# Kernel optimization log

Measured on AMD Instinct MI355X. Metric: run time of the kernel, lower is better.

Reference implementation:

```python
import jax, jax.numpy as jnp
import numpy as np

NUM_NODES = 100000
NUM_EDGES = 1600000
DIM = 64
TAU = 0.5
EPS = 1e-12
SURGERY_EPS = 1e-6


def setup_inputs() -> dict:
    key = jax.random.key(0)
    k1, k2, k3, k4, k5 = jax.random.split(key, 5)
    x = jax.random.normal(k1, (NUM_NODES, DIM), dtype=jnp.float32)
    edge_index = jax.random.randint(k2, (2, NUM_EDGES), 0, NUM_NODES, dtype=jnp.int64)
    edge_weight = jax.random.uniform(k3, (NUM_EDGES,), dtype=jnp.float32)
    # nn.Linear weights (no bias): y = x @ W.T
    W_self = jax.random.normal(k4, (DIM, DIM), dtype=jnp.float32) / np.sqrt(DIM)
    W_neigh = jax.random.normal(k5, (DIM, DIM), dtype=jnp.float32) / np.sqrt(DIM)
    return {"x": x, "edge_index": edge_index, "edge_weight": edge_weight,
            "W_self": W_self, "W_neigh": W_neigh}


def reference(x, edge_index, edge_weight, W_self, W_neigh):
    num_nodes = x.shape[0]
    row, col = edge_index[0], edge_index[1]

    # --- Ollivier-Ricci (LLY limit-free combinatorial lower-bound) curvature per edge ---
    deg = jax.ops.segment_sum(edge_weight, row, num_segments=num_nodes)  # weighted out-degree
    inv_du = 1.0 / jnp.maximum(deg[row], EPS)
    inv_dv = 1.0 / jnp.maximum(deg[col], EPS)
    kappa = 2.0 * inv_du + 2.0 * inv_dv - 2.0  # [E]

    # --- CFL-stable step size for the Ricci flow ---
    delta_t = 0.5 / (jnp.max(jnp.abs(kappa)) + 1e-6)

    # --- Ricci-flow half step: dw/dt = -kappa * w ---
    w_half = jnp.maximum(edge_weight * (1.0 - 0.5 * delta_t * kappa), 0.0)

    # --- metric surgery: drop degenerate edges (implemented as a zero-weight mask,
    #     keeping edge count static so the kernel is jit-compatible) ---
    mask = w_half > SURGERY_EPS
    w_half = jnp.where(mask, w_half, 0.0)

    # --- row normalisation ---
    row_sum = jax.ops.segment_sum(w_half, row, num_segments=num_nodes)
    w_norm = w_half / jnp.maximum(row_sum[row], EPS)

    # --- Laplacian off-diagonals: L_uv = -w_norm  =>  -L_uv = w_norm ---
    minus_L = w_norm

    # --- incident mean curvature per node (over surviving edges) -> curvature gate ---
    cnt = jax.ops.segment_sum(mask.astype(x.dtype), row, num_segments=num_nodes)
    k_sum = jax.ops.segment_sum(jnp.where(mask, kappa, 0.0), row, num_segments=num_nodes)
    mean_kappa = k_sum / jnp.maximum(cnt, 1.0)
    rho = jax.nn.sigmoid(mean_kappa)  # [N]

    # --- gated message passing ---
    h_self = x @ W_self.T    # [N, D]
    h_neigh = x @ W_neigh.T  # [N, D]
    msg = minus_L[:, None] * h_neigh[col]                      # [E, D] gather + scale
    neigh_aggr = jax.ops.segment_sum(msg, row, num_segments=num_nodes)  # scatter-add

    # h0 buffer == first-forward x (detached)
    out = rho[:, None] * h_self + neigh_aggr + TAU * x
    return out, edge_index, w_norm
```

## Files before the change

### kernel.cpp

```cpp
#include <hip/hip_runtime.h>
#include <math.h>

#define NNODES 100000
#define NEDGES 1600000
#define DIM 64
#define TAU 0.5f
#define EPSF 1e-12f
#define SEPS 1e-6f

#define K 256
#define RPB 391
#define TILE 8192
#define CAP 7168

typedef unsigned long long ull;
typedef unsigned short u16;
typedef __attribute__((ext_vector_type(8))) short bf16x8;
typedef __attribute__((ext_vector_type(4))) float f32x4;

__device__ __forceinline__ float bf2f(u16 h) {
    return __uint_as_float((unsigned)h << 16);
}
__device__ __forceinline__ u16 f2bf(float f) {
    unsigned u = __float_as_uint(f);
    u += 0x7FFFu + ((u >> 16) & 1);
    return (u16)(u >> 16);
}

__global__ __launch_bounds__(256) void k_bcount(const int* __restrict__ ei,
                                                int* __restrict__ bcnt, int E, int N) {
    __shared__ int cnt[K];
    cnt[threadIdx.x] = 0;
    __syncthreads();
    int stride = gridDim.x * blockDim.x;
    for (int e = blockIdx.x * blockDim.x + threadIdx.x; e < E; e += stride) {
        int r = min(max(ei[e], 0), N - 1);
        atomicAdd(&cnt[r / RPB], 1);
    }
    __syncthreads();
    int v = cnt[threadIdx.x];
    if (v) atomicAdd(&bcnt[threadIdx.x], v);
}

__global__ __launch_bounds__(256) void k_bscan(const int* __restrict__ bcnt,
                                               int* __restrict__ bbase, int* __restrict__ bcur,
                                               int* __restrict__ off, int E, int N) {
    __shared__ int sc[K];
    int t = threadIdx.x;
    int v = bcnt[t];
    sc[t] = v;
    __syncthreads();
    for (int o = 1; o < K; o <<= 1) {
        int a = (t >= o) ? sc[t - o] : 0;
        __syncthreads();
        sc[t] += a;
        __syncthreads();
    }
    int ex = sc[t] - v;
    bbase[t] = ex;
    bcur[t] = ex;
    if (t == K - 1) { bbase[K] = sc[t]; off[N] = E; }
}

__global__ __launch_bounds__(256) void k_bin(const int* __restrict__ ei, const float* __restrict__ w,
                                             int* __restrict__ bcur, ull* __restrict__ arena,
                                             int E, int N) {
    __shared__ ull stg[TILE];
    __shared__ int cnt[K], lscan[K], gbase[K], cur[K], sc[K];
    int t = threadIdx.x;
    int e0 = blockIdx.x * TILE;
    cnt[t] = 0; cur[t] = 0;
    __syncthreads();
    for (int i = t; i < TILE; i += 256) {
        int e = e0 + i;
        if (e < E) {
            int r = min(max(ei[e], 0), N - 1);
            atomicAdd(&cnt[r / RPB], 1);
        }
    }
    __syncthreads();
    int v = cnt[t];
    sc[t] = v;
    __syncthreads();
    for (int o = 1; o < K; o <<= 1) {
        int a = (t >= o) ? sc[t - o] : 0;
        __syncthreads();
        sc[t] += a;
        __syncthreads();
    }
    lscan[t] = sc[t] - v;
    if (v > 0) gbase[t] = atomicAdd(&bcur[t], v);
    __syncthreads();
    for (int i = t; i < TILE; i += 256) {
        int e = e0 + i;
        if (e < E) {
            int r = min(max(ei[e], 0), N - 1);
            int c = min(max(ei[E + e], 0), N - 1);
            int b = r / RPB, lr = r - b * RPB;
            int p = lscan[b] + atomicAdd(&cur[b], 1);
            stg[p] = ((ull)__float_as_uint(w[e]) << 32) | (unsigned)(c | (lr << 17));
        }
    }
    __syncthreads();
    int nb = cnt[t];
    if (nb > 0) {
        int src = lscan[t];
        size_t dst = (size_t)gbase[t];
        for (int j = 0; j < nb; j++) arena[dst + j] = stg[src + j];
    }
}

__global__ __launch_bounds__(256) void k_sort(const int* __restrict__ bbase,
                                              ull* __restrict__ arena,
                                              float* __restrict__ invdeg,
                                              int* __restrict__ off, int N) {
    __shared__ ull stg[CAP];
    __shared__ int hist[RPB];
    __shared__ float degl[RPB];
    __shared__ int cur[RPB];
    __shared__ int sc[512];
    int t = threadIdx.x, b = blockIdx.x;
    int base = bbase[b];
    int cnt = min(bbase[b + 1] - base, CAP);
    for (int i = t; i < RPB; i += 256) { hist[i] = 0; degl[i] = 0.0f; cur[i] = 0; }
    __syncthreads();
    for (int i = t; i < cnt; i += 256) {
        ull rec = arena[base + i];
        stg[i] = rec;
        int lr = (int)((rec >> 17) & 0x1FF);
        atomicAdd(&hist[lr], 1);
        atomicAdd(&degl[lr], __uint_as_float((unsigned)(rec >> 32)));
    }
    __syncthreads();
    int v0 = (t < RPB) ? hist[t] : 0;
    int v1 = (t + 256 < RPB) ? hist[t + 256] : 0;
    sc[t] = v0; sc[t + 256] = v1;
    __syncthreads();
    for (int o = 1; o < 512; o <<= 1) {
        int a = (t >= o) ? sc[t - o] : 0;
        int c2 = (t + 256 >= o) ? sc[t + 256 - o] : 0;
        __syncthreads();
        sc[t] += a; sc[t + 256] += c2;
        __syncthreads();
    }
    int ex0 = sc[t] - v0, ex1 = sc[t + 256] - v1;
    hist[t] = ex0;
    if (t + 256 < RPB) hist[t + 256] = ex1;
    int rn0 = b * RPB + t;
    if (rn0 < N) { off[rn0] = base + ex0; invdeg[rn0] = 1.0f / fmaxf(degl[t], EPSF); }
    int rn1 = rn0 + 256;
    if (t + 256 < RPB && rn1 < N) { off[rn1] = base + ex1; invdeg[rn1] = 1.0f / fmaxf(degl[t + 256], EPSF); }
    __syncthreads();
    int2* out2 = (int2*)arena;
    for (int i = t; i < cnt; i += 256) {
        ull rec = stg[i];
        int lr = (int)((rec >> 17) & 0x1FF);
        int p = hist[lr] + atomicAdd(&cur[lr], 1);
        out2[base + p] = make_int2((int)(rec & 0x1FFFF), (int)(unsigned)(rec >> 32));
    }
}

__global__ __launch_bounds__(256) void k_maxk(const int* __restrict__ off, const int2* __restrict__ csr,
                                              const float* __restrict__ invdeg,
                                              float* __restrict__ maxabs, int N) {
    int n = blockIdx.x * 256 + threadIdx.x;
    float m = 0.0f;
    if (n < N) {
        int s = off[n], e = off[n + 1];
        float a = 2.0f * invdeg[n] - 2.0f;
        for (int i = s; i < e; i++) {
            int2 pr = csr[i];
            m = fmaxf(m, fabsf(a + 2.0f * invdeg[pr.x]));
        }
    }
    for (int o = 32; o > 0; o >>= 1) m = fmaxf(m, __shfl_down(m, o, 64));
    __shared__ float red[4];
    int lane = threadIdx.x & 63, wid = threadIdx.x >> 6;
    if (lane == 0) red[wid] = m;
    __syncthreads();
    if (threadIdx.x == 0) {
        float bm = fmaxf(fmaxf(red[0], red[1]), fmaxf(red[2], red[3]));
        atomicMax((unsigned int*)maxabs, __float_as_uint(bm));
    }
}

__global__ void k_node(const int* __restrict__ off, const float* __restrict__ invdeg,
                       int2* __restrict__ csr, const float* __restrict__ maxabs,
                       float* __restrict__ rho, float* __restrict__ row_sum, int N) {
    int n = blockIdx.x * blockDim.x + threadIdx.x;
    if (n >= N) return;
    int s = off[n], e2 = off[n + 1];
    float dt = 0.5f / (*maxabs + 1e-6f);
    float a = 2.0f * invdeg[n] - 2.0f;
    float rs = 0.0f, ct = 0.0f, ks = 0.0f;
    for (int i = s; i < e2; i++) {
        int2 pr = csr[i];
        float we = __int_as_float(pr.y);
        float kap = a + 2.0f * invdeg[pr.x];
        float wh = fmaxf(we * (1.0f - 0.5f * dt * kap), 0.0f);
        float wst = 0.0f;
        if (wh > SEPS) { rs += wh; ct += 1.0f; ks += kap; wst = wh; }
        csr[i] = make_int2(pr.x, __float_as_int(wst));
    }
    float mk = ks / fmaxf(ct, 1.0f);
    rho[n] = 1.0f / (1.0f + expf(-mk));
    row_sum[n] = rs;
}

#define WL(mp, d, kk) (((mp) * 64 + (d)) * 72 + (kk))
__global__ __launch_bounds__(256) void k_gemm(const float* __restrict__ x,
                                              const float* __restrict__ Wself,
                                              const float* __restrict__ Wneigh,
                                              const float* __restrict__ rho,
                                              u16* __restrict__ hneigh_h,
                                              float* __restrict__ out, int N) {
    __shared__ u16 wlds[4 * 64 * 72];
    int t = threadIdx.x;
    for (int i = t; i < 4096; i += 256) {
        int d = i >> 6, k = i & 63;
        float v = Wself[i];
        u16 h = f2bf(v);
        u16 lo = f2bf(v - bf2f(h));
        wlds[WL(0, d, k)] = h;
        wlds[WL(1, d, k)] = lo;
        v = Wneigh[i];
        h = f2bf(v);
        lo = f2bf(v - bf2f(h));
        wlds[WL(2, d, k)] = h;
        wlds[WL(3, d, k)] = lo;
    }
    __syncthreads();
    int w = t >> 6, l = t & 63;
    int m = l & 15, kg = l >> 4;
    int n0 = blockIdx.x * 64 + w * 16;
    if (n0 >= N) return;
    int nodeA = n0 + m;
    bf16x8 ah[2], al[2];
#pragma unroll
    for (int ks = 0; ks < 2; ks++) {
        float v[8];
        if (nodeA < N) {
            const float4* xp = (const float4*)(x + (size_t)nodeA * 64 + ks * 32 + kg * 8);
            float4 v0 = xp[0], v1 = xp[1];
            v[0] = v0.x; v[1] = v0.y; v[2] = v0.z; v[3] = v0.w;
            v[4] = v1.x; v[5] = v1.y; v[6] = v1.z; v[7] = v1.w;
        } else {
#pragma unroll
            for (int j = 0; j < 8; j++) v[j] = 0.0f;
        }
#pragma unroll
        for (int j = 0; j < 8; j++) {
            u16 h = f2bf(v[j]);
            u16 lo = f2bf(v[j] - bf2f(h));
            ah[ks][j] = (short)h;
            al[ks][j] = (short)lo;
        }
    }
    f32x4 accS[4], accN[4];
#pragma unroll
    for (int dt = 0; dt < 4; dt++) {
        accS[dt] = (f32x4){0.0f, 0.0f, 0.0f, 0.0f};
        accN[dt] = (f32x4){0.0f, 0.0f, 0.0f, 0.0f};
    }
#pragma unroll
    for (int dt = 0; dt < 4; dt++) {
        int d = dt * 16 + m;
#pragma unroll
        for (int ks = 0; ks < 2; ks++) {
            int kof = ks * 32 + kg * 8;
            bf16x8 bsh = *(const bf16x8*)&wlds[WL(0, d, kof)];
            bf16x8 bsl = *(const bf16x8*)&wlds[WL(1, d, kof)];
            bf16x8 bnh = *(const bf16x8*)&wlds[WL(2, d, kof)];
            bf16x8 bnl = *(const bf16x8*)&wlds[WL(3, d, kof)];
            accS[dt] = __builtin_amdgcn_mfma_f32_16x16x32_bf16(ah[ks], bsh, accS[dt], 0, 0, 0);
            accS[dt] = __builtin_amdgcn_mfma_f32_16x16x32_bf16(al[ks], bsh, accS[dt], 0, 0, 0);
            accS[dt] = __builtin_amdgcn_mfma_f32_16x16x32_bf16(ah[ks], bsl, accS[dt], 0, 0, 0);
            accN[dt] = __builtin_amdgcn_mfma_f32_16x16x32_bf16(ah[ks], bnh, accN[dt], 0, 0, 0);
            accN[dt] = __builtin_amdgcn_mfma_f32_16x16x32_bf16(al[ks], bnh, accN[dt], 0, 0, 0);
            accN[dt] = __builtin_amdgcn_mfma_f32_16x16x32_bf16(ah[ks], bnl, accN[dt], 0, 0, 0);
        }
    }
    int rbase = kg * 4;
#pragma unroll
    for (int r = 0; r < 4; r++) {
        int nn = n0 + rbase + r;
        if (nn >= N) continue;
        float rh = rho[nn];
#pragma unroll
        for (int dt = 0; dt < 4; dt++) {
            int d = dt * 16 + m;
            size_t idx = (size_t)nn * 64 + d;
            out[idx] = rh * accS[dt][r] + TAU * x[idx];
            hneigh_h[idx] = f2bf(accN[dt][r]);
        }
    }
}

__global__ __launch_bounds__(256) void k_aggr(const int* __restrict__ off,
                                              const int2* __restrict__ csr,
                                              const float* __restrict__ row_sum,
                                              const u16* __restrict__ hneigh_h,
                                              float* __restrict__ out, int N) {
    int t = threadIdx.x;
    int lane = t & 63;
    int q = lane & 15;
    int g = lane >> 4;
    int n = blockIdx.x * 4 + (t >> 6);
    if (n >= N) return;
    int s = off[n], end = off[n + 1];
    float inv_rs = 1.0f / fmaxf(row_sum[n], EPSF);
    const ushort4* hn4 = (const ushort4*)hneigh_h;
    float a0 = 0.0f, a1 = 0.0f, a2 = 0.0f, a3 = 0.0f;
    int i = s;
    for (; i + 16 <= end; i += 16) {
        int2 p0 = csr[i + g];
        int2 p1 = csr[i + 4 + g];
        int2 p2 = csr[i + 8 + g];
        int2 p3 = csr[i + 12 + g];
        ushort4 h0 = hn4[(unsigned)((p0.x << 4) | q)];
        ushort4 h1 = hn4[(unsigned)((p1.x << 4) | q)];
        ushort4 h2 = hn4[(unsigned)((p2.x << 4) | q)];
        ushort4 h3 = hn4[(unsigned)((p3.x << 4) | q)];
        float w0 = __int_as_float(p0.y), w1 = __int_as_float(p1.y);
        float w2 = __int_as_float(p2.y), w3 = __int_as_float(p3.y);
        a0 = fmaf(w0, bf2f(h0.x), a0); a1 = fmaf(w0, bf2f(h0.y), a1);
        a2 = fmaf(w0, bf2f(h0.z), a2); a3 = fmaf(w0, bf2f(h0.w), a3);
        a0 = fmaf(w1, bf2f(h1.x), a0); a1 = fmaf(w1, bf2f(h1.y), a1);
        a2 = fmaf(w1, bf2f(h1.z), a2); a3 = fmaf(w1, bf2f(h1.w), a3);
        a0 = fmaf(w2, bf2f(h2.x), a0); a1 = fmaf(w2, bf2f(h2.y), a1);
        a2 = fmaf(w2, bf2f(h2.z), a2); a3 = fmaf(w2, bf2f(h2.w), a3);
        a0 = fmaf(w3, bf2f(h3.x), a0); a1 = fmaf(w3, bf2f(h3.y), a1);
        a2 = fmaf(w3, bf2f(h3.z), a2); a3 = fmaf(w3, bf2f(h3.w), a3);
    }
    for (; i + 8 <= end; i += 8) {
        int2 p0 = csr[i + g];
        int2 p1 = csr[i + 4 + g];
        ushort4 h0 = hn4[(unsigned)((p0.x << 4) | q)];
        ushort4 h1 = hn4[(unsigned)((p1.x << 4) | q)];
        float w0 = __int_as_float(p0.y), w1 = __int_as_float(p1.y);
        a0 = fmaf(w0, bf2f(h0.x), a0); a1 = fmaf(w0, bf2f(h0.y), a1);
        a2 = fmaf(w0, bf2f(h0.z), a2); a3 = fmaf(w0, bf2f(h0.w), a3);
        a0 = fmaf(w1, bf2f(h1.x), a0); a1 = fmaf(w1, bf2f(h1.y), a1);
        a2 = fmaf(w1, bf2f(h1.z), a2); a3 = fmaf(w1, bf2f(h1.w), a3);
    }
    for (; i < end; i += 4) {
        int e = i + g;
        bool v = e < end;
        int2 p = make_int2(0, 0);
        if (v) p = csr[e];
        ushort4 h = hn4[(unsigned)((p.x << 4) | q)];
        float wv = v ? __int_as_float(p.y) : 0.0f;
        a0 = fmaf(wv, bf2f(h.x), a0);
        a1 = fmaf(wv, bf2f(h.y), a1);
        a2 = fmaf(wv, bf2f(h.z), a2);
        a3 = fmaf(wv, bf2f(h.w), a3);
    }
    a0 += __shfl_xor(a0, 16, 64);
    a1 += __shfl_xor(a1, 16, 64);
    a2 += __shfl_xor(a2, 16, 64);
    a3 += __shfl_xor(a3, 16, 64);
    a0 += __shfl_xor(a0, 32, 64);
    a1 += __shfl_xor(a1, 32, 64);
    a2 += __shfl_xor(a2, 32, 64);
    a3 += __shfl_xor(a3, 32, 64);
    if (g == 0) {
        float4* o4 = (float4*)(out + (size_t)n * 64);
        float4 o = o4[q];
        o.x += a0 * inv_rs;
        o.y += a1 * inv_rs;
        o.z += a2 * inv_rs;
        o.w += a3 * inv_rs;
        o4[q] = o;
    }
}

__global__ void k_final(const int* __restrict__ ei, const float* __restrict__ w,
                        const float* __restrict__ invdeg, const float* __restrict__ row_sum,
                        const float* __restrict__ maxabs,
                        float* __restrict__ out_ei, float* __restrict__ out_wn, int E, int N) {
    int e = blockIdx.x * blockDim.x + threadIdx.x;
    if (e >= E) return;
    int r0 = ei[e], c0 = ei[E + e];
    int r = min(max(r0, 0), N - 1);
    int c = min(max(c0, 0), N - 1);
    float dt = 0.5f / (*maxabs + 1e-6f);
    float kap = 2.0f * invdeg[r] + 2.0f * invdeg[c] - 2.0f;
    float wh = fmaxf(w[e] * (1.0f - 0.5f * dt * kap), 0.0f);
    if (wh <= SEPS) wh = 0.0f;
    out_wn[e] = wh / fmaxf(row_sum[r], EPSF);
    out_ei[e] = (float)r0;
    out_ei[E + e] = (float)c0;
}

extern "C" void kernel_launch(void* const* d_in, const int* in_sizes, int n_in,
                              void* d_out, int out_size, void* d_ws, size_t ws_size,
                              hipStream_t stream) {
    (void)in_sizes; (void)n_in; (void)out_size; (void)ws_size;
    const int N = NNODES, E = NEDGES;

    const float* x      = (const float*)d_in[0];
    const int*   ei     = (const int*)d_in[1];
    const float* w      = (const float*)d_in[2];
    const float* Wself  = (const float*)d_in[3];
    const float* Wneigh = (const float*)d_in[4];

    float* out    = (float*)d_out;
    float* out_ei = out + (size_t)N * DIM;
    float* out_wn = out_ei + 2 * (size_t)E;

    ull*  arena = (ull*)out_ei;
    int2* csr   = (int2*)out_ei;

    float* invdeg  = (float*)d_ws;
    int*   off     = (int*)d_ws + (size_t)N;
    float* rho     = (float*)d_ws + 2 * (size_t)N + 16;
    float* row_sum = rho + (size_t)N;
    float* maxabs  = row_sum + (size_t)N;
    int*   bcnt    = (int*)(maxabs + 4);
    int*   bbase   = bcnt + 256;
    int*   bcur    = bbase + 257;
    u16*   hneigh_h = (u16*)((float*)d_ws + 4 * (size_t)N + 800);

    hipMemsetAsync((void*)maxabs, 0, 260 * sizeof(float), stream);

    k_bcount<<<256, 256, 0, stream>>>(ei, bcnt, E, N);
    k_bscan<<<1, 256, 0, stream>>>(bcnt, bbase, bcur, off, E, N);
    k_bin<<<(E + TILE - 1) / TILE, 256, 0, stream>>>(ei, w, bcur, arena, E, N);
    k_sort<<<K, 256, 0, stream>>>(bbase, arena, invdeg, off, N);
    k_maxk<<<(N + 255) / 256, 256, 0, stream>>>(off, csr, invdeg, maxabs, N);
    k_node<<<(N + 255) / 256, 256, 0, stream>>>(off, invdeg, csr, maxabs, rho, row_sum, N);
    k_gemm<<<(N + 63) / 64, 256, 0, stream>>>(x, Wself, Wneigh, rho, hneigh_h, out, N);
    k_aggr<<<(N + 3) / 4, 256, 0, stream>>>(off, csr, row_sum, hneigh_h, out, N);
    k_final<<<(E + 255) / 256, 256, 0, stream>>>(ei, w, invdeg, row_sum, maxabs,
                                                 out_ei, out_wn, E, N);
}
```

Baseline: 295.9 us.

## Register-cache edge records in binning kernel and coalesce arena flush

The binning kernel now loads each edge's row, column and weight once into per-thread registers (16 per thread), instead of reading the row index twice across two passes. The tile size is halved, and a per-slot bucket byte is stored in shared memory. The final copy to the global arena becomes a thread-strided loop over all staged entries rather than one thread serially copying a whole bucket. This targets redundant global reads and the poorly coalesced, load-imbalanced write-out, at the cost of more registers, more blocks, and more global atomics on the bucket cursors.

Measured after the change: 279.7 us. -5.5%, faster.

```diff
diff --git a/kernel.cpp b/kernel.cpp
--- a/kernel.cpp
+++ b/kernel.cpp
@@ -10,7 +10,8 @@
 
 #define K 256
 #define RPB 391
-#define TILE 8192
+#define TILE 4096
+#define EPT 16
 #define CAP 7168
 
 typedef unsigned long long ull;
@@ -66,47 +67,56 @@
                                              int* __restrict__ bcur, ull* __restrict__ arena,
                                              int E, int N) {
     __shared__ ull stg[TILE];
+    __shared__ unsigned char bkt[TILE];
     __shared__ int cnt[K], lscan[K], gbase[K], cur[K], sc[K];
+    __shared__ int tot;
     int t = threadIdx.x;
     int e0 = blockIdx.x * TILE;
     cnt[t] = 0; cur[t] = 0;
     __syncthreads();
-    for (int i = t; i < TILE; i += 256) {
-        int e = e0 + i;
-        if (e < E) {
-            int r = min(max(ei[e], 0), N - 1);
-            atomicAdd(&cnt[r / RPB], 1);
-        }
-    }
-    __syncthreads();
-    int v = cnt[t];
-    sc[t] = v;
-    __syncthreads();
-    for (int o = 1; o < K; o <<= 1) {
-        int a = (t >= o) ? sc[t - o] : 0;
-        __syncthreads();
-        sc[t] += a;
-        __syncthreads();
-    }
-    lscan[t] = sc[t] - v;
-    if (v > 0) gbase[t] = atomicAdd(&bcur[t], v);
-    __syncthreads();
-    for (int i = t; i < TILE; i += 256) {
-        int e = e0 + i;
+    ull rec[EPT];
+    int bb[EPT];
+#pragma unroll
+    for (int j = 0; j < EPT; j++) {
+        int e = e0 + t + j * 256;
+        bb[j] = -1;
         if (e < E) {
             int r = min(max(ei[e], 0), N - 1);
             int c = min(max(ei[E + e], 0), N - 1);
+            float wv = w[e];
             int b = r / RPB, lr = r - b * RPB;
-            int p = lscan[b] + atomicAdd(&cur[b], 1);
-            stg[p] = ((ull)__float_as_uint(w[e]) << 32) | (unsigned)(c | (lr << 17));
-        }
-    }
-    __syncthreads();
-    int nb = cnt[t];
-    if (nb > 0) {
-        int src = lscan[t];
-        size_t dst = (size_t)gbase[t];
-        for (int j = 0; j < nb; j++) arena[dst + j] = stg[src + j];
+            rec[j] = ((ull)__float_as_uint(wv) << 32) | (unsigned)(c | (lr << 17));
+            bb[j] = b;
+            atomicAdd(&cnt[b], 1);
+        }
+    }
+    __syncthreads();
+    int v = cnt[t];
+    sc[t] = v;
+    __syncthreads();
+    for (int o = 1; o < K; o <<= 1) {
+        int a = (t >= o) ? sc[t - o] : 0;
+        __syncthreads();
+        sc[t] += a;
+        __syncthreads();
+    }
+    lscan[t] = sc[t] - v;
+    if (v > 0) gbase[t] = atomicAdd(&bcur[t], v);
+    if (t == K - 1) tot = sc[t];
+    __syncthreads();
+#pragma unroll
+    for (int j = 0; j < EPT; j++) {
+        if (bb[j] >= 0) {
+            int p = lscan[bb[j]] + atomicAdd(&cur[bb[j]], 1);
+            stg[p] = rec[j];
+            bkt[p] = (unsigned char)bb[j];
+        }
+    }
+    __syncthreads();
+    int T = tot;
+    for (int i = t; i < T; i += 256) {
+        int b = bkt[i];
+        arena[(size_t)gbase[b] + (i - lscan[b])] = stg[i];
     }
 }
 
```
